# Kernel tuning notes

Hardware: AMD Instinct MI355X
Metric: run time of the kernel (lower is better)

## Reference

```python
import jax, jax.numpy as jnp
import numpy as np

NUM_HEADS = 16
ROPE_THETA = 10000.0


def setup_inputs() -> dict:
    key = jax.random.key(0)
    k1, k2, k3 = jax.random.split(key, 3)
    B, S, D = 2, 2048, 1024
    std_qkv = float(np.sqrt(2.0 / (D + 3 * D)))
    std_out = float(np.sqrt(2.0 / (D + D)))
    return {
        "x": jax.random.normal(k1, (B, S, D), dtype=jnp.float32),
        "qkv_w": jax.random.normal(k2, (3 * D, D), dtype=jnp.float32) * std_qkv,
        "out_w": jax.random.normal(k3, (D, D), dtype=jnp.float32) * std_out,
        "token_positions": jnp.arange(S, dtype=jnp.int32),
    }


def _apply_rope(x, token_positions, theta=ROPE_THETA):
    # x: [B, H, S, d_k], token_positions: [S]
    d_k = x.shape[-1]
    inv_freqs = 1.0 / (theta ** (jnp.arange(0, d_k, 2, dtype=jnp.float32) / d_k))  # [d_k/2]
    angles = token_positions.astype(jnp.float32)[:, None] * inv_freqs[None, :]     # [S, d_k/2]
    cos, sin = jnp.cos(angles), jnp.sin(angles)
    x_even, x_odd = x[..., 0::2], x[..., 1::2]
    r_even = x_even * cos - x_odd * sin
    r_odd = x_even * sin + x_odd * cos
    # interleave back: [..., d_k/2, 2] -> [..., d_k]
    return jnp.stack([r_even, r_odd], axis=-1).reshape(x.shape)


def reference(x, qkv_w, out_w, token_positions):
    B, S, D = x.shape
    H = NUM_HEADS
    d_k = D // H

    qkv = jnp.einsum("bsd,ed->bse", x, qkv_w)                  # [B, S, 3*D]
    qkv = qkv.reshape(B, S, 3, H, d_k)
    q, k, v = (jnp.transpose(qkv[:, :, i], (0, 2, 1, 3)) for i in range(3))  # each [B, H, S, d_k]

    q = _apply_rope(q, token_positions)
    k = _apply_rope(k, token_positions)

    scale = 1.0 / jnp.sqrt(jnp.asarray(d_k, dtype=x.dtype))
    scores = jnp.einsum("bhqd,bhkd->bhqk", q, k) * scale       # [B, H, S, S]
    causal = jnp.tril(jnp.ones((S, S), dtype=bool))
    scores = jnp.where(causal, scores, jnp.asarray(-jnp.inf, dtype=scores.dtype))
    attn = jax.nn.softmax(scores, axis=-1)
    out = jnp.einsum("bhqk,bhkd->bhqd", attn, v)               # [B, H, S, d_k]
    out = jnp.transpose(out, (0, 2, 1, 3)).reshape(B, S, D)    # [B, S, D]
    return jnp.einsum("bsd,ed->bse", out, out_w)               # [B, S, D]
```

## Files before the change

### kernel.cpp

```cpp
#include <hip/hip_runtime.h>

typedef __bf16 bf16x8 __attribute__((ext_vector_type(8)));
typedef float f32x4 __attribute__((ext_vector_type(4)));
typedef unsigned short u16;
typedef u16 u16x8 __attribute__((ext_vector_type(8)));
typedef u16 u16x2 __attribute__((ext_vector_type(2)));

__device__ __forceinline__ u16 f2bf(float f) {
    union { float f; unsigned u; } x; x.f = f;
    unsigned r = x.u + 0x7fffu + ((x.u >> 16) & 1u);
    return (u16)(r >> 16);
}
__device__ __forceinline__ float bf2f(u16 v) {
    union { unsigned u; float f; } x; x.u = ((unsigned)v) << 16;
    return x.f;
}
__device__ __forceinline__ bf16x8 as_bf16x8(u16x8 v) {
    return __builtin_bit_cast(bf16x8, v);
}
__device__ __forceinline__ void glds16(const void* g, void* l) {
    __builtin_amdgcn_global_load_lds(
        (const __attribute__((address_space(1))) void*)g,
        (__attribute__((address_space(3))) void*)l, 16, 0, 0);
}
__device__ __forceinline__ int swz(int r) { return (((r & 7) ^ ((r >> 3) & 7)) << 3); }

__global__ __launch_bounds__(256) void f32bf16(const float* __restrict__ in,
                                               u16* __restrict__ out, int n8) {
    int i = blockIdx.x * 256 + threadIdx.x;
    if (i >= n8) return;
    const float4* p = (const float4*)(in + (size_t)i * 8);
    float4 a = p[0], b = p[1];
    u16x8 o;
    o[0] = f2bf(a.x); o[1] = f2bf(a.y); o[2] = f2bf(a.z); o[3] = f2bf(a.w);
    o[4] = f2bf(b.x); o[5] = f2bf(b.y); o[6] = f2bf(b.z); o[7] = f2bf(b.w);
    *(u16x8*)(out + (size_t)i * 8) = o;
}

template<bool BF16OUT>
__global__ __launch_bounds__(256) void gemm128(const u16* __restrict__ A,
                                               const u16* __restrict__ B,
                                               void* __restrict__ Cv,
                                               int N, int K, int nbx) {
    __shared__ u16 As[2][4096];
    __shared__ u16 Bs[2][4096];
    const int tid = threadIdx.x, lane = tid & 63, wave = tid >> 6;
    const int cpx = gridDim.x >> 3;
    const int nid = (blockIdx.x & 7) * cpx + (blockIdx.x >> 3);
    const int m0 = (nid / nbx) << 7, n0 = (nid % nbx) << 7;
    const int wr = (wave >> 1) << 6, wc = (wave & 1) << 6;
    const int fr = lane & 15, fo = (lane >> 4) << 3;
    const int srow = tid >> 2, scol = (tid & 3) << 3;
    const u16* Ag = A + (size_t)(m0 + srow) * K + scol;
    const u16* Bg = B + (size_t)(n0 + srow) * K + scol;
    u16* AsW = &As[0][0] + (wave << 9);
    u16* BsW = &Bs[0][0] + (wave << 9);
    f32x4 acc[4][4] = {};
    const int nsteps = K >> 5;
    glds16(Ag, AsW);
    glds16(Ag + (size_t)64 * K, AsW + 2048);
    glds16(Bg, BsW);
    glds16(Bg + (size_t)64 * K, BsW + 2048);
    int cur = 0;
    for (int s = 0; s < nsteps; ++s) {
        __syncthreads();
        if (s + 1 < nsteps) {
            const u16* Ap = Ag + (s + 1) * 32;
            const u16* Bp = Bg + (s + 1) * 32;
            const int nb = (cur ^ 1) << 12;
            glds16(Ap, AsW + nb);
            glds16(Ap + (size_t)64 * K, AsW + nb + 2048);
            glds16(Bp, BsW + nb);
            glds16(Bp + (size_t)64 * K, BsW + nb + 2048);
        }
        const u16* Ab = &As[cur][0];
        const u16* Bb = &Bs[cur][0];
        bf16x8 af[4], bfr[4];
        #pragma unroll
        for (int i = 0; i < 4; ++i)
            af[i] = *(const bf16x8*)(Ab + (wr + i * 16 + fr) * 32 + fo);
        #pragma unroll
        for (int i = 0; i < 4; ++i)
            bfr[i] = *(const bf16x8*)(Bb + (wc + i * 16 + fr) * 32 + fo);
        #pragma unroll
        for (int i = 0; i < 4; ++i)
            #pragma unroll
            for (int j = 0; j < 4; ++j)
                acc[i][j] = __builtin_amdgcn_mfma_f32_16x16x32_bf16(af[i], bfr[j], acc[i][j], 0, 0, 0);
        cur ^= 1;
    }
    const int cr = (lane >> 4) << 2, cc = lane & 15;
    if constexpr (BF16OUT) {
        u16* C = (u16*)Cv;
        #pragma unroll
        for (int i = 0; i < 4; ++i)
            for (int j = 0; j < 4; ++j)
                for (int r = 0; r < 4; ++r)
                    C[(size_t)(m0 + wr + i * 16 + cr + r) * N + (n0 + wc + j * 16 + cc)] =
                        f2bf(acc[i][j][r]);
    } else {
        float* C = (float*)Cv;
        #pragma unroll
        for (int i = 0; i < 4; ++i)
            for (int j = 0; j < 4; ++j)
                for (int r = 0; r < 4; ++r)
                    C[(size_t)(m0 + wr + i * 16 + cr + r) * N + (n0 + wc + j * 16 + cc)] =
                        acc[i][j][r];
    }
}

__global__ __launch_bounds__(256) void rope_split(const u16* __restrict__ qkv,
                                                  const int* __restrict__ pos,
                                                  u16* __restrict__ Qb,
                                                  u16* __restrict__ Kb) {
    int tid = blockIdx.x * 256 + threadIdx.x;
    int t = tid & 31;
    int h = (tid >> 5) & 15;
    int s = (tid >> 9) & 2047;
    int b = tid >> 20;
    const u16* row = qkv + (size_t)((b << 11) + s) * 3072;
    float fp  = (float)pos[s];
    float inv = exp2f((float)t * -0.4152410118609203f);
    float rev = fp * inv * 0.15915494309189535f;
    rev = rev - floorf(rev);
    float sn = __builtin_amdgcn_sinf(rev);
    float cs = __builtin_amdgcn_cosf(rev);
    int off = h * 64 + 2 * t;
    u16x2 q2 = *(const u16x2*)(row + off);
    u16x2 k2 = *(const u16x2*)(row + 1024 + off);
    float qx = bf2f(q2[0]), qy = bf2f(q2[1]);
    float kx = bf2f(k2[0]), ky = bf2f(k2[1]);
    size_t oidx = (((size_t)(b * 16 + h) * 2048) + s) * 64 + 2 * t;
    const float qs = 0.18033688011112042f;
    u16x2 qo, ko;
    qo[0] = f2bf((qx * cs - qy * sn) * qs);
    qo[1] = f2bf((qx * sn + qy * cs) * qs);
    ko[0] = f2bf(kx * cs - ky * sn);
    ko[1] = f2bf(ky * cs + kx * sn);
    *(u16x2*)&Qb[oidx] = qo;
    *(u16x2*)&Kb[oidx] = ko;
}

__global__ __launch_bounds__(256) void vtrans(const u16* __restrict__ qkv,
                                              u16* __restrict__ Vt) {
    __shared__ u16 lds[64][72];
    const int t = threadIdx.x;
    const int st = blockIdx.x, h = blockIdx.y, b = blockIdx.z;
    const int s0 = st << 6;
    {
        const int r = t >> 2, c0 = (t & 3) << 4;
        const u16* src = qkv + (size_t)((b << 11) + s0 + r) * 3072 + 2048 + h * 64 + c0;
        *(u16x8*)&lds[r][c0]     = *(const u16x8*)src;
        *(u16x8*)&lds[r][c0 + 8] = *(const u16x8*)(src + 8);
    }
    __syncthreads();
    const size_t obase = ((size_t)((b << 4) + h) << 17) + (st << 6);
    #pragma unroll
    for (int w = 0; w < 2; ++w) {
        const int q = t + (w << 8);
        const int d = q >> 3, c = q & 7;
        u16x8 o;
        #pragma unroll
        for (int i = 0; i < 8; ++i) {
            const int p = (c << 3) + i;
            const int k = ((p >> 5) << 5) + (((p >> 3) & 3) << 2) + (p & 3)
                        + (((p >> 2) & 1) << 4);
            o[i] = lds[k][d];
        }
        *(u16x8*)(Vt + obase + ((size_t)d << 11) + (c << 3)) = o;
    }
}

__global__ __launch_bounds__(512, 4) void attn_causal(const u16* __restrict__ Q,
                                                      const u16* __restrict__ K,
                                                      const u16* __restrict__ Vt,
                                                      u16* __restrict__ O) {
    __shared__ u16 smem[24576];
    __shared__ float cmb[5120];
    const int tid = threadIdx.x, lane = tid & 63, wave = tid >> 6;
    const int nid = ((blockIdx.x & 7) << 6) + (blockIdx.x >> 3);
    const int pr = nid & 15, h = (nid >> 4) & 15, b = nid >> 8;
    const int S = 2048;
    const size_t base = (size_t)((b << 4) + h) << 17;
    const int fr = lane & 15, fo = (lane >> 4) << 3, cr = (lane >> 4) << 2;
    const int schk = lane & 7, srow8 = lane >> 3;
    const int qsub = wave >> 1, half = wave & 1;
    float* const slot = cmb + qsub * 1280 + lane * 20;
    u16x8 ones_u;
    #pragma unroll
    for (int i = 0; i < 8; ++i) ones_u[i] = 0x3F80;
    const bf16x8 ones = as_bf16x8(ones_u);

    auto stage = [&](int t, int bi) {
        const int r  = (wave << 3) + srow8;
        const int ck = (schk ^ srow8 ^ wave) << 3;
        glds16(K  + base + ((size_t)((t << 6) + r) << 6) + ck,
               &smem[bi * 8192 + (wave << 9)]);
        glds16(Vt + base + ((size_t)r << 11) + (t << 6) + ck,
               &smem[bi * 8192 + 4096 + (wave << 9)]);
    };

    for (int phase = 0; phase < 2; ++phase) {
        const int qt = phase ? (31 - pr) : pr;
        const int nkt = qt + 1;
        const int qw = (qt << 6) + (qsub << 4);
        bf16x8 aq0, aq1;
        {
            const u16* qrow = Q + base + (size_t)(qw + fr) * 64;
            aq0 = as_bf16x8(*(const u16x8*)(qrow + fo));
            aq1 = as_bf16x8(*(const u16x8*)(qrow + 32 + fo));
        }
        f32x4 oacc[4] = {};
        f32x4 lacc = {};
        const int qloc = (qsub << 4) + fr;
        stage(0, 0);
        if (nkt > 1) stage(1, 1);
        int cur = 0;
        for (int t = 0; t < nkt; ++t) {
            if (t + 1 < nkt) asm volatile("s_waitcnt vmcnt(2)" ::: "memory");
            else             asm volatile("s_waitcnt vmcnt(0)" ::: "memory");
            __builtin_amdgcn_s_barrier();
            __builtin_amdgcn_sched_barrier(0);
            int nb = cur + 2; if (nb >= 3) nb -= 3;
            if (t + 2 < nkt) stage(t + 2, nb);
            const u16* Kb = smem + cur * 8192;
            const u16* Vb = smem + cur * 8192 + 4096;
            const bool diag = (t == nkt - 1);
            f32x4 sacc[2];
            #pragma unroll
            for (int ch = 0; ch < 2; ++ch) {
                const int r = ((half << 1) + ch) * 16 + fr;
                const int sw = swz(r);
                bf16x8 bk0 = *(const bf16x8*)&Kb[r * 64 + (fo ^ sw)];
                bf16x8 bk1 = *(const bf16x8*)&Kb[r * 64 + ((32 + fo) ^ sw)];
                f32x4 sc = {};
                sc = __builtin_amdgcn_mfma_f32_16x16x32_bf16(bk0, aq0, sc, 0, 0, 0);
                sc = __builtin_amdgcn_mfma_f32_16x16x32_bf16(bk1, aq1, sc, 0, 0, 0);
                sacc[ch] = sc;
            }
            bf16x8 pa;
            #pragma unroll
            for (int ch = 0; ch < 2; ++ch) {
                const int cglob = (half << 1) + ch;
                #pragma unroll
                for (int r = 0; r < 4; ++r) {
                    float e = exp2f(sacc[ch][r]);
                    if (diag) {
                        const int kloc = (cglob << 4) + cr + r;
                        e = (kloc <= qloc) ? e : 0.f;
                    }
                    pa[ch * 4 + r] = (__bf16)e;
                }
            }
            lacc = __builtin_amdgcn_mfma_f32_16x16x32_bf16(pa, ones, lacc, 0, 0, 0);
            #pragma unroll
            for (int tt = 0; tt < 4; ++tt) {
                const int d = tt * 16 + fr;
                bf16x8 bv = *(const bf16x8*)&Vb[d * 64 + (((half << 5) + fo) ^ swz(d))];
                oacc[tt] = __builtin_amdgcn_mfma_f32_16x16x32_bf16(pa, bv, oacc[tt], 0, 0, 0);
            }
            cur = (cur + 1 == 3) ? 0 : cur + 1;
        }
        __syncthreads();
        if (half) {
            #pragma unroll
            for (int tt = 0; tt < 4; ++tt) *(f32x4*)(slot + tt * 4) = oacc[tt];
            *(f32x4*)(slot + 16) = lacc;
        }
        __syncthreads();
        if (!half) {
            #pragma unroll
            for (int tt = 0; tt < 4; ++tt) oacc[tt] += *(const f32x4*)(slot + tt * 4);
            lacc += *(const f32x4*)(slot + 16);
            f32x4 inv;
            #pragma unroll
            for (int j = 0; j < 4; ++j) inv[j] = 1.f / lacc[j];
            #pragma unroll
            for (int tt = 0; tt < 4; ++tt)
                for (int j = 0; j < 4; ++j)
                    O[(size_t)(b * S + qw + cr + j) * 1024 + h * 64 + tt * 16 + fr] =
                        f2bf(oacc[tt][j] * inv[j]);
        }
        __syncthreads();
    }
}

extern "C" void kernel_launch(void* const* d_in, const int* in_sizes, int n_in,
                              void* d_out, int out_size, void* d_ws, size_t ws_size,
                              hipStream_t stream) {
    const float* x     = (const float*)d_in[0];
    const float* qkv_w = (const float*)d_in[1];
    const float* out_w = (const float*)d_in[2];
    const int*   pos   = (const int*)d_in[3];
    float* out = (float*)d_out;

    char* ws = (char*)d_ws;
    u16* qkv16 = (u16*)ws;
    u16* Qb    = (u16*)(ws + 25165824);
    u16* Kb    = (u16*)(ws + 33554432);
    u16* Vtg   = (u16*)(ws + 41943040);
    u16* x16   = (u16*)(ws + 50331648);
    u16* att16 = (u16*)(ws + 50331648);
    u16* w16   = (u16*)(ws + 58720256);
    u16* ow16  = (u16*)(ws + 65011712);

    f32bf16<<<2048, 256, 0, stream>>>(x, x16, 524288);
    f32bf16<<<1536, 256, 0, stream>>>(qkv_w, w16, 393216);
    f32bf16<<<512, 256, 0, stream>>>(out_w, ow16, 131072);
    gemm128<true><<<768, 256, 0, stream>>>(x16, w16, (void*)qkv16, 3072, 1024, 24);
    rope_split<<<8192, 256, 0, stream>>>(qkv16, pos, Qb, Kb);
    vtrans<<<dim3(32, 16, 2), 256, 0, stream>>>(qkv16, Vtg);
    attn_causal<<<512, 512, 0, stream>>>(Qb, Kb, Vtg, att16);
    gemm128<false><<<256, 256, 0, stream>>>(att16, ow16, (void*)out, 1024, 1024, 8);
}
```

Baseline: 121.9 us.

## Merge conversion and rope/vtrans launches; give each attention wave two query groups

The three fp32-to-bf16 conversions now run as a single kernel, and rope and the V transpose share one launch, which cuts the number of kernel launches. The attention kernel moves to 256-thread blocks where each wave handles two 16-row query groups against the same K/V fragments. This reuses LDS reads of K and V across more MFMAs, and each thread now stages two chunks per tile. s_setprio hints are added around the MFMA sections. The risks are higher register pressure, fewer waves per CU to hide latency, and a larger LDS combine buffer.

```diff
diff --git a/kernel.cpp b/kernel.cpp
--- a/kernel.cpp
+++ b/kernel.cpp
@@ -25,16 +25,23 @@
 }
 __device__ __forceinline__ int swz(int r) { return (((r & 7) ^ ((r >> 3) & 7)) << 3); }
 
-__global__ __launch_bounds__(256) void f32bf16(const float* __restrict__ in,
-                                               u16* __restrict__ out, int n8) {
+__global__ __launch_bounds__(256) void cvt3(const float* __restrict__ x,
+                                            const float* __restrict__ w,
+                                            const float* __restrict__ ow,
+                                            u16* __restrict__ x16,
+                                            u16* __restrict__ w16,
+                                            u16* __restrict__ ow16) {
     int i = blockIdx.x * 256 + threadIdx.x;
-    if (i >= n8) return;
-    const float4* p = (const float4*)(in + (size_t)i * 8);
+    const float* in; u16* out; int off;
+    if (i < 524288)       { in = x;  out = x16;  off = i; }
+    else if (i < 917504)  { in = w;  out = w16;  off = i - 524288; }
+    else                  { in = ow; out = ow16; off = i - 917504; }
+    const float4* p = (const float4*)(in + (size_t)off * 8);
     float4 a = p[0], b = p[1];
     u16x8 o;
     o[0] = f2bf(a.x); o[1] = f2bf(a.y); o[2] = f2bf(a.z); o[3] = f2bf(a.w);
     o[4] = f2bf(b.x); o[5] = f2bf(b.y); o[6] = f2bf(b.z); o[7] = f2bf(b.w);
-    *(u16x8*)(out + (size_t)i * 8) = o;
+    *(u16x8*)(out + (size_t)off * 8) = o;
 }
 
 template<bool BF16OUT>
@@ -109,74 +116,75 @@
     }
 }
 
-__global__ __launch_bounds__(256) void rope_split(const u16* __restrict__ qkv,
-                                                  const int* __restrict__ pos,
-                                                  u16* __restrict__ Qb,
-                                                  u16* __restrict__ Kb) {
-    int tid = blockIdx.x * 256 + threadIdx.x;
-    int t = tid & 31;
-    int h = (tid >> 5) & 15;
-    int s = (tid >> 9) & 2047;
-    int b = tid >> 20;
-    const u16* row = qkv + (size_t)((b << 11) + s) * 3072;
-    float fp  = (float)pos[s];
-    float inv = exp2f((float)t * -0.4152410118609203f);
-    float rev = fp * inv * 0.15915494309189535f;
-    rev = rev - floorf(rev);
-    float sn = __builtin_amdgcn_sinf(rev);
-    float cs = __builtin_amdgcn_cosf(rev);
-    int off = h * 64 + 2 * t;
-    u16x2 q2 = *(const u16x2*)(row + off);
-    u16x2 k2 = *(const u16x2*)(row + 1024 + off);
-    float qx = bf2f(q2[0]), qy = bf2f(q2[1]);
-    float kx = bf2f(k2[0]), ky = bf2f(k2[1]);
-    size_t oidx = (((size_t)(b * 16 + h) * 2048) + s) * 64 + 2 * t;
-    const float qs = 0.18033688011112042f;
-    u16x2 qo, ko;
-    qo[0] = f2bf((qx * cs - qy * sn) * qs);
-    qo[1] = f2bf((qx * sn + qy * cs) * qs);
-    ko[0] = f2bf(kx * cs - ky * sn);
-    ko[1] = f2bf(ky * cs + kx * sn);
-    *(u16x2*)&Qb[oidx] = qo;
-    *(u16x2*)&Kb[oidx] = ko;
-}
-
-__global__ __launch_bounds__(256) void vtrans(const u16* __restrict__ qkv,
-                                              u16* __restrict__ Vt) {
+__global__ __launch_bounds__(256) void rope_vt(const u16* __restrict__ qkv,
+                                               const int* __restrict__ pos,
+                                               u16* __restrict__ Qb,
+                                               u16* __restrict__ Kb,
+                                               u16* __restrict__ Vt) {
     __shared__ u16 lds[64][72];
-    const int t = threadIdx.x;
-    const int st = blockIdx.x, h = blockIdx.y, b = blockIdx.z;
-    const int s0 = st << 6;
-    {
-        const int r = t >> 2, c0 = (t & 3) << 4;
-        const u16* src = qkv + (size_t)((b << 11) + s0 + r) * 3072 + 2048 + h * 64 + c0;
-        *(u16x8*)&lds[r][c0]     = *(const u16x8*)src;
-        *(u16x8*)&lds[r][c0 + 8] = *(const u16x8*)(src + 8);
+    if (blockIdx.x < 8192) {
+        int tid = blockIdx.x * 256 + threadIdx.x;
+        int t = tid & 31;
+        int h = (tid >> 5) & 15;
+        int s = (tid >> 9) & 2047;
+        int b = tid >> 20;
+        const u16* row = qkv + (size_t)((b << 11) + s) * 3072;
+        float fp  = (float)pos[s];
+        float inv = exp2f((float)t * -0.4152410118609203f);
+        float rev = fp * inv * 0.15915494309189535f;
+        rev = rev - floorf(rev);
+        float sn = __builtin_amdgcn_sinf(rev);
+        float cs = __builtin_amdgcn_cosf(rev);
+        int off = h * 64 + 2 * t;
+        u16x2 q2 = *(const u16x2*)(row + off);
+        u16x2 k2 = *(const u16x2*)(row + 1024 + off);
+        float qx = bf2f(q2[0]), qy = bf2f(q2[1]);
+        float kx = bf2f(k2[0]), ky = bf2f(k2[1]);
+        size_t oidx = (((size_t)(b * 16 + h) * 2048) + s) * 64 + 2 * t;
+        const float qs = 0.18033688011112042f;
+        u16x2 qo, ko;
+        qo[0] = f2bf((qx * cs - qy * sn) * qs);
+        qo[1] = f2bf((qx * sn + qy * cs) * qs);
+        ko[0] = f2bf(kx * cs - ky * sn);
+        ko[1] = f2bf(ky * cs + kx * sn);
+        *(u16x2*)&Qb[oidx] = qo;
+        *(u16x2*)&Kb[oidx] = ko;
+    } else {
+        const int idx = blockIdx.x - 8192;
+        const int t = threadIdx.x;
+        const int st = idx & 31, h = (idx >> 5) & 15, b = idx >> 9;
+        const int s0 = st << 6;
+        {
+            const int r = t >> 2, c0 = (t & 3) << 4;
+            const u16* src = qkv + (size_t)((b << 11) + s0 + r) * 3072 + 2048 + h * 64 + c0;
+            *(u16x8*)&lds[r][c0]     = *(const u16x8*)src;
+            *(u16x8*)&lds[r][c0 + 8] = *(const u16x8*)(src + 8);
+        }
+        __syncthreads();
+        const size_t obase = ((size_t)((b << 4) + h) << 17) + (st << 6);
+        #pragma unroll
+        for (int w = 0; w < 2; ++w) {
+            const int q = t + (w << 8);
+            const int d = q >> 3, c = q & 7;
+            u16x8 o;
+            #pragma unroll
+            for (int i = 0; i < 8; ++i) {
+                const int p = (c << 3) + i;
+                const int k = ((p >> 5) << 5) + (((p >> 3) & 3) << 2) + (p & 3)
+                            + (((p >> 2) & 1) << 4);
+                o[i] = lds[k][d];
+            }
+            *(u16x8*)(Vt + obase + ((size_t)d << 11) + (c << 3)) = o;
+        }
     }
-    __syncthreads();
-    const size_t obase = ((size_t)((b << 4) + h) << 17) + (st << 6);
-    #pragma unroll
-    for (int w = 0; w < 2; ++w) {
-        const int q = t + (w << 8);
-        const int d = q >> 3, c = q & 7;
-        u16x8 o;
-        #pragma unroll
-        for (int i = 0; i < 8; ++i) {
-            const int p = (c << 3) + i;
-            const int k = ((p >> 5) << 5) + (((p >> 3) & 3) << 2) + (p & 3)
-                        + (((p >> 2) & 1) << 4);
-            o[i] = lds[k][d];
-        }
-        *(u16x8*)(Vt + obase + ((size_t)d << 11) + (c << 3)) = o;
-    }
-}
-
-__global__ __launch_bounds__(512, 4) void attn_causal(const u16* __restrict__ Q,
+}
+
+__global__ __launch_bounds__(256, 2) void attn_causal(const u16* __restrict__ Q,
                                                       const u16* __restrict__ K,
                                                       const u16* __restrict__ Vt,
                                                       u16* __restrict__ O) {
     __shared__ u16 smem[24576];
-    __shared__ float cmb[5120];
+    __shared__ float cmb[5248];
     const int tid = threadIdx.x, lane = tid & 63, wave = tid >> 6;
     const int nid = ((blockIdx.x & 7) << 6) + (blockIdx.x >> 3);
     const int pr = nid & 15, h = (nid >> 4) & 15, b = nid >> 8;
@@ -185,39 +193,43 @@
     const int fr = lane & 15, fo = (lane >> 4) << 3, cr = (lane >> 4) << 2;
     const int schk = lane & 7, srow8 = lane >> 3;
     const int qsub = wave >> 1, half = wave & 1;
-    float* const slot = cmb + qsub * 1280 + lane * 20;
+    float* const slot = cmb + qsub * 2624 + lane * 41;
     u16x8 ones_u;
     #pragma unroll
     for (int i = 0; i < 8; ++i) ones_u[i] = 0x3F80;
     const bf16x8 ones = as_bf16x8(ones_u);
 
     auto stage = [&](int t, int bi) {
-        const int r  = (wave << 3) + srow8;
-        const int ck = (schk ^ srow8 ^ wave) << 3;
-        glds16(K  + base + ((size_t)((t << 6) + r) << 6) + ck,
-               &smem[bi * 8192 + (wave << 9)]);
-        glds16(Vt + base + ((size_t)r << 11) + (t << 6) + ck,
-               &smem[bi * 8192 + 4096 + (wave << 9)]);
+        #pragma unroll
+        for (int g = 0; g < 2; ++g) {
+            const int rg = (wave << 1) + g;
+            const int r  = (rg << 3) + srow8;
+            const int ck = (schk ^ srow8 ^ rg) << 3;
+            glds16(K  + base + ((size_t)((t << 6) + r) << 6) + ck,
+                   &smem[bi * 8192 + (rg << 9)]);
+            glds16(Vt + base + ((size_t)r << 11) + (t << 6) + ck,
+                   &smem[bi * 8192 + 4096 + (rg << 9)]);
+        }
     };
 
     for (int phase = 0; phase < 2; ++phase) {
         const int qt = phase ? (31 - pr) : pr;
         const int nkt = qt + 1;
-        const int qw = (qt << 6) + (qsub << 4);
-        bf16x8 aq0, aq1;
-        {
-            const u16* qrow = Q + base + (size_t)(qw + fr) * 64;
-            aq0 = as_bf16x8(*(const u16x8*)(qrow + fo));
-            aq1 = as_bf16x8(*(const u16x8*)(qrow + 32 + fo));
-        }
-        f32x4 oacc[4] = {};
-        f32x4 lacc = {};
-        const int qloc = (qsub << 4) + fr;
+        const int qw = (qt << 6) + (qsub << 5);
+        bf16x8 aq[2][2];
+        #pragma unroll
+        for (int qg = 0; qg < 2; ++qg) {
+            const u16* qrow = Q + base + (size_t)(qw + (qg << 4) + fr) * 64;
+            aq[qg][0] = as_bf16x8(*(const u16x8*)(qrow + fo));
+            aq[qg][1] = as_bf16x8(*(const u16x8*)(qrow + 32 + fo));
+        }
+        f32x4 oacc[2][4] = {};
+        f32x4 lacc[2] = {};
         stage(0, 0);
         if (nkt > 1) stage(1, 1);
         int cur = 0;
         for (int t = 0; t < nkt; ++t) {
-            if (t + 1 < nkt) asm volatile("s_waitcnt vmcnt(2)" ::: "memory");
+            if (t + 1 < nkt) asm volatile("s_waitcnt vmcnt(4)" ::: "memory");
             else             asm volatile("s_waitcnt vmcnt(0)" ::: "memory");
             __builtin_amdgcn_s_barrier();
             __builtin_amdgcn_sched_barrier(0);
@@ -226,60 +238,80 @@
             const u16* Kb = smem + cur * 8192;
             const u16* Vb = smem + cur * 8192 + 4096;
             const bool diag = (t == nkt - 1);
-            f32x4 sacc[2];
+            f32x4 sacc[2][2];
+            __builtin_amdgcn_s_setprio(1);
             #pragma unroll
             for (int ch = 0; ch < 2; ++ch) {
                 const int r = ((half << 1) + ch) * 16 + fr;
                 const int sw = swz(r);
                 bf16x8 bk0 = *(const bf16x8*)&Kb[r * 64 + (fo ^ sw)];
                 bf16x8 bk1 = *(const bf16x8*)&Kb[r * 64 + ((32 + fo) ^ sw)];
-                f32x4 sc = {};
-                sc = __builtin_amdgcn_mfma_f32_16x16x32_bf16(bk0, aq0, sc, 0, 0, 0);
-                sc = __builtin_amdgcn_mfma_f32_16x16x32_bf16(bk1, aq1, sc, 0, 0, 0);
-                sacc[ch] = sc;
-            }
-            bf16x8 pa;
-            #pragma unroll
-            for (int ch = 0; ch < 2; ++ch) {
-                const int cglob = (half << 1) + ch;
-                #pragma unroll
-                for (int r = 0; r < 4; ++r) {
-                    float e = exp2f(sacc[ch][r]);
-                    if (diag) {
-                        const int kloc = (cglob << 4) + cr + r;
-                        e = (kloc <= qloc) ? e : 0.f;
+                #pragma unroll
+                for (int qg = 0; qg < 2; ++qg) {
+                    f32x4 sc = {};
+                    sc = __builtin_amdgcn_mfma_f32_16x16x32_bf16(bk0, aq[qg][0], sc, 0, 0, 0);
+                    sc = __builtin_amdgcn_mfma_f32_16x16x32_bf16(bk1, aq[qg][1], sc, 0, 0, 0);
+                    sacc[qg][ch] = sc;
+                }
+            }
+            __builtin_amdgcn_s_setprio(0);
+            bf16x8 pa[2];
+            #pragma unroll
+            for (int qg = 0; qg < 2; ++qg) {
+                const int qloc = (qsub << 5) + (qg << 4) + fr;
+                #pragma unroll
+                for (int ch = 0; ch < 2; ++ch) {
+                    const int cglob = (half << 1) + ch;
+                    #pragma unroll
+                    for (int r = 0; r < 4; ++r) {
+                        float e = exp2f(sacc[qg][ch][r]);
+                        if (diag) {
+                            const int kloc = (cglob << 4) + cr + r;
+                            e = (kloc <= qloc) ? e : 0.f;
+                        }
+                        pa[qg][ch * 4 + r] = (__bf16)e;
                     }
-                    pa[ch * 4 + r] = (__bf16)e;
                 }
             }
-            lacc = __builtin_amdgcn_mfma_f32_16x16x32_bf16(pa, ones, lacc, 0, 0, 0);
+            __builtin_amdgcn_s_setprio(1);
+            lacc[0] = __builtin_amdgcn_mfma_f32_16x16x32_bf16(pa[0], ones, lacc[0], 0, 0, 0);
+            lacc[1] = __builtin_amdgcn_mfma_f32_16x16x32_bf16(pa[1], ones, lacc[1], 0, 0, 0);
             #pragma unroll
             for (int tt = 0; tt < 4; ++tt) {
                 const int d = tt * 16 + fr;
                 bf16x8 bv = *(const bf16x8*)&Vb[d * 64 + (((half << 5) + fo) ^ swz(d))];
-                oacc[tt] = __builtin_amdgcn_mfma_f32_16x16x32_bf16(pa, bv, oacc[tt], 0, 0, 0);
-            }
+                oacc[0][tt] = __builtin_amdgcn_mfma_f32_16x16x32_bf16(pa[0], bv, oacc[0][tt], 0, 0, 0);
+                oacc[1][tt] = __builtin_amdgcn_mfma_f32_16x16x32_bf16(pa[1], bv, oacc[1][tt], 0, 0, 0);
+            }
+            __builtin_amdgcn_s_setprio(0);
             cur = (cur + 1 == 3) ? 0 : cur + 1;
         }
         __syncthreads();
         if (half) {
             #pragma unroll
-            for (int tt = 0; tt < 4; ++tt) *(f32x4*)(slot + tt * 4) = oacc[tt];
-            *(f32x4*)(slot + 16) = lacc;
+            for (int qg = 0; qg < 2; ++qg) {
+                #pragma unroll
+                for (int tt = 0; tt < 4; ++tt)
+                    *(f32x4*)(slot + (qg * 4 + tt) * 4) = oacc[qg][tt];
+                *(f32x4*)(slot + 32 + qg * 4) = lacc[qg];
+            }
         }
         __syncthreads();
         if (!half) {
             #pragma unroll
-            for (int tt = 0; tt < 4; ++tt) oacc[tt] += *(const f32x4*)(slot + tt * 4);
-            lacc += *(const f32x4*)(slot + 16);
-            f32x4 inv;
-            #pragma unroll
-            for (int j = 0; j < 4; ++j) inv[j] = 1.f / lacc[j];
-            #pragma unroll
-            for (int tt = 0; tt < 4; ++tt)
-                for (int j = 0; j < 4; ++j)
-                    O[(size_t)(b * S + qw + cr + j) * 1024 + h * 64 + tt * 16 + fr] =
-                        f2bf(oacc[tt][j] * inv[j]);
+            for (int qg = 0; qg < 2; ++qg) {
+                #pragma unroll
+                for (int tt = 0; tt < 4; ++tt) oacc[qg][tt] += *(const f32x4*)(slot + (qg * 4 + tt) * 4);
+                lacc[qg] += *(const f32x4*)(slot + 32 + qg * 4);
+                f32x4 inv;
+                #pragma unroll
+                for (int j = 0; j < 4; ++j) inv[j] = 1.f / lacc[qg][j];
+                #pragma unroll
+                for (int tt = 0; tt < 4; ++tt)
+                    for (int j = 0; j < 4; ++j)
+                        O[(size_t)(b * S + qw + (qg << 4) + cr + j) * 1024 + h * 64 + tt * 16 + fr] =
+                            f2bf(oacc[qg][tt][j] * inv[j]);
+            }
         }
         __syncthreads();
     }
@@ -304,12 +336,9 @@
     u16* w16   = (u16*)(ws + 58720256);
     u16* ow16  = (u16*)(ws + 65011712);
 
-    f32bf16<<<2048, 256, 0, stream>>>(x, x16, 524288);
-    f32bf16<<<1536, 256, 0, stream>>>(qkv_w, w16, 393216);
-    f32bf16<<<512, 256, 0, stream>>>(out_w, ow16, 131072);
+    cvt3<<<4096, 256, 0, stream>>>(x, qkv_w, out_w, x16, w16, ow16);
     gemm128<true><<<768, 256, 0, stream>>>(x16, w16, (void*)qkv16, 3072, 1024, 24);
-    rope_split<<<8192, 256, 0, stream>>>(qkv16, pos, Qb, Kb);
-    vtrans<<<dim3(32, 16, 2), 256, 0, stream>>>(qkv16, Vtg);
-    attn_causal<<<512, 512, 0, stream>>>(Qb, Kb, Vtg, att16);
+    rope_vt<<<9216, 256, 0, stream>>>(qkv16, pos, Qb, Kb, Vtg);
+    attn_causal<<<512, 256, 0, stream>>>(Qb, Kb, Vtg, att16);
     gemm128<false><<<256, 256, 0, stream>>>(att16, ow16, (void*)out, 1024, 1024, 8);
 }
```

Result: faster. 118.6 us (-2.7%).
